# Optimization experiments

Measured on AMD Instinct MI355X. Metric: run time of the kernel, lower is better.

## Reference

```python
import jax, jax.numpy as jnp
import numpy as np

EMD_DIM = 64
NB_EMD = 512


def setup_inputs() -> dict:
    key = jax.random.key(0)
    k_x, k_e = jax.random.split(key)
    x = jax.random.normal(k_x, (32, 64, 64, EMD_DIM), dtype=jnp.float32)
    # codebook buffer, shape [emd_dim, nb_emd] as in the torch module
    embed = jax.random.normal(k_e, (EMD_DIM, NB_EMD), dtype=jnp.float32)
    return {"x": x, "embed": embed}


def reference(x, embed):
    # Eval-mode forward (the EMA buffer update only runs under self.training
    # and does not affect this forward's outputs).
    flatten = x.reshape(-1, EMD_DIM)                      # [N, d]
    dist = (jnp.sum(flatten * flatten, axis=1, keepdims=True)
            - 2.0 * flatten @ embed
            + jnp.sum(embed * embed, axis=0, keepdims=True))  # [N, K]
    emd_id_flat = jnp.argmax(-dist, axis=1)               # nearest code index [N]
    emd_id = emd_id_flat.reshape(x.shape[:-1])            # [B, H, W]
    q = jnp.take(embed.T, emd_id, axis=0)                 # gather codes -> [B,H,W,d]
    diff = jnp.mean((jax.lax.stop_gradient(q) - x) ** 2)  # commitment loss
    q_st = x + jax.lax.stop_gradient(q - x)               # straight-through
    return (q_st, diff, emd_id)
```

## Files before the change

kernel.cpp:

```cpp
#include <hip/hip_runtime.h>

#define N_VEC 131072
#define D 64
#define K 512
#define GUARD 0.05f
#define NB_GATHER 2048
#define FB_Q 16

typedef __attribute__((ext_vector_type(8))) short bf16x8;
typedef __attribute__((ext_vector_type(4))) float f32x4;

static __device__ __forceinline__ short f2bf(float f) {
  unsigned u = __builtin_bit_cast(unsigned, f);
  u += 0x7fffu + ((u >> 16) & 1u);
  return (short)(u >> 16);
}
static __device__ __forceinline__ float bf2f(short h) {
  unsigned u = ((unsigned)(unsigned short)h) << 16;
  return __builtin_bit_cast(float, u);
}
static __device__ __forceinline__ void split8(const float4 f0, const float4 f1,
                                              bf16x8& h, bf16x8& m) {
  const float v[8] = {f0.x, f0.y, f0.z, f0.w, f1.x, f1.y, f1.z, f1.w};
#pragma unroll
  for (int j = 0; j < 8; ++j) {
    const short hh = f2bf(v[j]);
    h[j] = hh;
    m[j] = f2bf(v[j] - bf2f(hh));
  }
}

__global__ __launch_bounds__(64) void vq_prep_kernel(
    const float* __restrict__ embed, float* __restrict__ et,
    float* __restrict__ nrm, bf16x8* __restrict__ F, int* __restrict__ cnt)
{
  const int b = blockIdx.x;
  const int lane = threadIdx.x;
  if (b < 32) {
    const int row = lane & 15;
    const int kg  = lane >> 4;
    const int code = b * 16 + row;
#pragma unroll
    for (int c = 0; c < 2; ++c) {
      bf16x8 h, m;
#pragma unroll
      for (int j = 0; j < 8; ++j) {
        const int d = kg * 8 + c * 32 + j;
        const float e = embed[d * K + code];
        const short hh = f2bf(e);
        h[j] = hh;
        m[j] = f2bf(e - bf2f(hh));
      }
      F[b * 256 + c * 128 + 0  + lane] = h;
      F[b * 256 + c * 128 + 64 + lane] = m;
    }
  } else {
    if (b == 32 && lane == 0) cnt[0] = 0;
    const int code = (b - 32) * 64 + lane;
    float s = 0.f;
#pragma unroll
    for (int d = 0; d < D; ++d) {
      const float e = embed[d * K + code];
      et[code * D + d] = e;
      s = fmaf(e, e, s);
    }
    nrm[code] = s;
  }
}

__global__ __launch_bounds__(64, 4) void vq_coarse_kernel(
    const float* __restrict__ x, const bf16x8* __restrict__ F,
    const float* __restrict__ nrm, float* __restrict__ idf,
    int* __restrict__ cnt, int* __restrict__ list)
{
  const int lane = threadIdx.x;
  const int wid  = blockIdx.x;
  const int qbase = wid * 32;
  const int row = lane & 15;
  const int kg  = lane >> 4;

  bf16x8 Ah0c0, Ah0c1, Ah1c0, Ah1c1, Am0c0, Am0c1, Am1c0, Am1c1;
  {
    const float* xr0 = x + (size_t)(qbase + row) * D + kg * 8;
    const float* xr1 = x + (size_t)(qbase + 16 + row) * D + kg * 8;
    split8(*reinterpret_cast<const float4*>(xr0),
           *reinterpret_cast<const float4*>(xr0 + 4), Ah0c0, Am0c0);
    split8(*reinterpret_cast<const float4*>(xr0 + 32),
           *reinterpret_cast<const float4*>(xr0 + 36), Ah0c1, Am0c1);
    split8(*reinterpret_cast<const float4*>(xr1),
           *reinterpret_cast<const float4*>(xr1 + 4), Ah1c0, Am1c0);
    split8(*reinterpret_cast<const float4*>(xr1 + 32),
           *reinterpret_cast<const float4*>(xr1 + 36), Ah1c1, Am1c1);
  }

  float b1[8], b2[8]; int i1[8];
#pragma unroll
  for (int r = 0; r < 8; ++r) { b1[r] = 3.4e38f; b2[r] = 3.4e38f; i1[r] = 0; }

  const bf16x8* fp = F + lane;
  bf16x8 Bh0 = fp[0], Bm0 = fp[64], Bh1 = fp[128], Bm1 = fp[192];
  fp += 256;
  const float* np = nrm + row;
  float nv = np[0];
  np += 16;

#pragma unroll 1
  for (int t = 0; t < 32; ++t) {
    bf16x8 nh0, nm0, nh1, nm1; float nvn;
    if (t < 31) {
      nh0 = fp[0]; nm0 = fp[64]; nh1 = fp[128]; nm1 = fp[192]; fp += 256;
      nvn = np[0]; np += 16;
    }

    f32x4 p0 = {0.f,0.f,0.f,0.f}, q0 = {0.f,0.f,0.f,0.f};
    f32x4 p1 = {0.f,0.f,0.f,0.f}, q1 = {0.f,0.f,0.f,0.f};
    p0 = __builtin_amdgcn_mfma_f32_16x16x32_bf16(Ah0c0, Bh0, p0, 0, 0, 0);
    p1 = __builtin_amdgcn_mfma_f32_16x16x32_bf16(Ah1c0, Bh0, p1, 0, 0, 0);
    q0 = __builtin_amdgcn_mfma_f32_16x16x32_bf16(Ah0c1, Bm1, q0, 0, 0, 0);
    q1 = __builtin_amdgcn_mfma_f32_16x16x32_bf16(Ah1c1, Bm1, q1, 0, 0, 0);
    p0 = __builtin_amdgcn_mfma_f32_16x16x32_bf16(Ah0c1, Bh1, p0, 0, 0, 0);
    p1 = __builtin_amdgcn_mfma_f32_16x16x32_bf16(Ah1c1, Bh1, p1, 0, 0, 0);
    q0 = __builtin_amdgcn_mfma_f32_16x16x32_bf16(Am0c0, Bh0, q0, 0, 0, 0);
    q1 = __builtin_amdgcn_mfma_f32_16x16x32_bf16(Am1c0, Bh0, q1, 0, 0, 0);
    p0 = __builtin_amdgcn_mfma_f32_16x16x32_bf16(Ah0c0, Bm0, p0, 0, 0, 0);
    p1 = __builtin_amdgcn_mfma_f32_16x16x32_bf16(Ah1c0, Bm0, p1, 0, 0, 0);
    q0 = __builtin_amdgcn_mfma_f32_16x16x32_bf16(Am0c1, Bh1, q0, 0, 0, 0);
    q1 = __builtin_amdgcn_mfma_f32_16x16x32_bf16(Am1c1, Bh1, q1, 0, 0, 0);

    const int code = t * 16 + row;
#pragma unroll
    for (int r = 0; r < 4; ++r) {
      const float s0 = fmaf(-2.f, p0[r], fmaf(-2.f, q0[r], nv));
      b2[r] = __builtin_amdgcn_fmed3f(s0, b1[r], b2[r]);
      if (s0 < b1[r]) { b1[r] = s0; i1[r] = code; }
      const float s1 = fmaf(-2.f, p1[r], fmaf(-2.f, q1[r], nv));
      b2[4 + r] = __builtin_amdgcn_fmed3f(s1, b1[4 + r], b2[4 + r]);
      if (s1 < b1[4 + r]) { b1[4 + r] = s1; i1[4 + r] = code; }
    }
    Bh0 = nh0; Bm0 = nm0; Bh1 = nh1; Bm1 = nm1; nv = nvn;
  }

#pragma unroll
  for (int m = 1; m < 16; m <<= 1) {
#pragma unroll
    for (int r = 0; r < 8; ++r) {
      const float o1 = __shfl_xor(b1[r], m, 64);
      const int   oi = __shfl_xor(i1[r], m, 64);
      const float o2 = __shfl_xor(b2[r], m, 64);
      if (o1 < b1[r]) { b2[r] = fminf(b1[r], o2); b1[r] = o1; i1[r] = oi; }
      else            { b2[r] = fminf(b2[r], o1); }
    }
  }

  unsigned m32 = 0;
  if (row == 0) {
#pragma unroll
    for (int r = 0; r < 8; ++r) {
      const int qoff = (r >> 2) * 16 + kg * 4 + (r & 3);
      idf[qbase + qoff] = (float)i1[r];
      if (b2[r] - b1[r] < GUARD) m32 |= 1u << qoff;
    }
  }
  m32 |= __shfl_xor((int)m32, 16, 64);
  m32 |= __shfl_xor((int)m32, 32, 64);
  if (lane == 0 && m32) {
    int base = atomicAdd(cnt, __popc(m32));
    while (m32) {
      const int b = __ffs(m32) - 1;
      m32 &= m32 - 1;
      list[base++] = qbase + b;
    }
  }
}

__global__ __launch_bounds__(256) void vq_fallback_kernel(
    const float* __restrict__ x, const float* __restrict__ embed,
    const float* __restrict__ nrm, const int* __restrict__ cnt,
    const int* __restrict__ list, float* __restrict__ idf)
{
  __shared__ float x_lds[FB_Q * D];
  __shared__ int   s_qidx[FB_Q];
  __shared__ float s_best[4][FB_Q];
  __shared__ int   s_bid[4][FB_Q];
  const int tid  = threadIdx.x;
  const int lane = tid & 63;
  const int wv   = tid >> 6;
  const int n = cnt[0];

  for (int qb = blockIdx.x * FB_Q; qb < n; qb += gridDim.x * FB_Q) {
    __syncthreads();
    if (tid < FB_Q) {
      const int idx = qb + tid;
      s_qidx[tid] = list[idx < n ? idx : qb];
    }
    __syncthreads();
    {
      const int qj = tid >> 4, dq = tid & 15;
      *reinterpret_cast<float4*>(&x_lds[qj * D + dq * 4]) =
          *reinterpret_cast<const float4*>(x + (size_t)s_qidx[qj] * D + dq * 4);
    }
    __syncthreads();

    const int c0 = wv * 128 + lane;
    const int c1 = c0 + 64;
    float a0[FB_Q], a1[FB_Q];
#pragma unroll
    for (int i = 0; i < FB_Q; ++i) { a0[i] = 0.f; a1[i] = 0.f; }

#pragma unroll 4
    for (int ch = 0; ch < 16; ++ch) {
      const int d0 = ch * 4;
      const float e00 = embed[(d0 + 0) * K + c0];
      const float e01 = embed[(d0 + 0) * K + c1];
      const float e10 = embed[(d0 + 1) * K + c0];
      const float e11 = embed[(d0 + 1) * K + c1];
      const float e20 = embed[(d0 + 2) * K + c0];
      const float e21 = embed[(d0 + 2) * K + c1];
      const float e30 = embed[(d0 + 3) * K + c0];
      const float e31 = embed[(d0 + 3) * K + c1];
#pragma unroll
      for (int i = 0; i < FB_Q; ++i) {
        const float4 xv = *reinterpret_cast<const float4*>(&x_lds[i * D + d0]);
        a0[i] = fmaf(xv.x, e00, a0[i]);
        a0[i] = fmaf(xv.y, e10, a0[i]);
        a0[i] = fmaf(xv.z, e20, a0[i]);
        a0[i] = fmaf(xv.w, e30, a0[i]);
        a1[i] = fmaf(xv.x, e01, a1[i]);
        a1[i] = fmaf(xv.y, e11, a1[i]);
        a1[i] = fmaf(xv.z, e21, a1[i]);
        a1[i] = fmaf(xv.w, e31, a1[i]);
      }
    }

    const float nr0 = nrm[c0], nr1 = nrm[c1];
#pragma unroll
    for (int i = 0; i < FB_Q; ++i) {
      float best; int bid;
      const float s0 = fmaf(-2.f, a0[i], nr0);
      best = s0; bid = c0;
      const float s1 = fmaf(-2.f, a1[i], nr1);
      if (s1 < best) { best = s1; bid = c1; }
#pragma unroll
      for (int off = 32; off > 0; off >>= 1) {
        const float s2 = __shfl_down(best, off, 64);
        const int   b2 = __shfl_down(bid, off, 64);
        if (s2 < best || (s2 == best && b2 < bid)) { best = s2; bid = b2; }
      }
      if (lane == 0) { s_best[wv][i] = best; s_bid[wv][i] = bid; }
    }
    __syncthreads();
    if (tid < FB_Q) {
      float best = s_best[0][tid]; int bid = s_bid[0][tid];
#pragma unroll
      for (int w = 1; w < 4; ++w) {
        const float s = s_best[w][tid];
        if (s < best) { best = s; bid = s_bid[w][tid]; }
      }
      idf[s_qidx[tid]] = (float)bid;
    }
  }
}

__global__ __launch_bounds__(256) void vq_gather_kernel(
    const float* __restrict__ x, const float* __restrict__ et,
    const float* __restrict__ idf, float* __restrict__ q,
    float* __restrict__ partial)
{
  const int tid = blockIdx.x * 256 + threadIdx.x;
  const int stride = gridDim.x * 256;
  float acc = 0.f;
  for (int idx = tid; idx < N_VEC * (D / 4); idx += stride) {
    const int v = idx >> 4;
    const int d4 = idx & 15;
    const int id = (int)idf[v];
    const float4 xv = reinterpret_cast<const float4*>(x)[idx];
    const float4 ev = reinterpret_cast<const float4*>(et)[(id << 4) + d4];
    const float e0 = ev.x - xv.x, e1 = ev.y - xv.y, e2 = ev.z - xv.z, e3 = ev.w - xv.w;
    acc += (e0 * e0 + e1 * e1) + (e2 * e2 + e3 * e3);
    reinterpret_cast<float4*>(q)[idx] = ev;
  }
  acc += __shfl_down(acc, 32, 64);
  acc += __shfl_down(acc, 16, 64);
  acc += __shfl_down(acc, 8, 64);
  acc += __shfl_down(acc, 4, 64);
  acc += __shfl_down(acc, 2, 64);
  acc += __shfl_down(acc, 1, 64);
  __shared__ float sred[4];
  if ((threadIdx.x & 63) == 0) sred[threadIdx.x >> 6] = acc;
  __syncthreads();
  if (threadIdx.x == 0)
    partial[blockIdx.x] = (sred[0] + sred[1]) + (sred[2] + sred[3]);
}

__global__ __launch_bounds__(256) void vq_finalize_kernel(
    const float* __restrict__ partial, float* __restrict__ out)
{
  float acc = 0.f;
  for (int i = threadIdx.x; i < NB_GATHER; i += 256) acc += partial[i];
  acc += __shfl_down(acc, 32, 64);
  acc += __shfl_down(acc, 16, 64);
  acc += __shfl_down(acc, 8, 64);
  acc += __shfl_down(acc, 4, 64);
  acc += __shfl_down(acc, 2, 64);
  acc += __shfl_down(acc, 1, 64);
  __shared__ float sred[4];
  if ((threadIdx.x & 63) == 0) sred[threadIdx.x >> 6] = acc;
  __syncthreads();
  if (threadIdx.x == 0)
    out[0] = ((sred[0] + sred[1]) + (sred[2] + sred[3])) * (1.0f / (float)(N_VEC * D));
}

extern "C" void kernel_launch(void* const* d_in, const int* in_sizes, int n_in,
                              void* d_out, int out_size, void* d_ws, size_t ws_size,
                              hipStream_t stream) {
  const float* x = (const float*)d_in[0];
  const float* embed = (const float*)d_in[1];
  float* out = (float*)d_out;
  float* q    = out;
  float* diff = out + 8388608;
  float* idf  = out + 8388609;

  float* ws = (float*)d_ws;
  float* et      = ws;
  float* nrm     = ws + 32768;
  float* partial = ws + 33280;
  int*   cnt     = (int*)(ws + 35328);
  int*   list    = (int*)(ws + 35336);
  bf16x8* F = (bf16x8*)(ws + 35336 + N_VEC);

  vq_prep_kernel<<<40, 64, 0, stream>>>(embed, et, nrm, F, cnt);
  vq_coarse_kernel<<<N_VEC / 32, 64, 0, stream>>>(x, F, nrm, idf, cnt, list);
  vq_fallback_kernel<<<1024, 256, 0, stream>>>(x, embed, nrm, cnt, list, idf);
  vq_gather_kernel<<<NB_GATHER, 256, 0, stream>>>(x, et, idf, q, partial);
  vq_finalize_kernel<<<1, 256, 0, stream>>>(partial, diff);
}
```

Baseline: 84.67 us.

## Software-pipeline coarse MFMA distance tiles with double-buffered accumulators

The coarse search loop is unrolled by two, with two sets of accumulators and codebook fragment registers. The MFMAs for the next 16-code tile are issued while the VALU scores and updates the top-2 for the previous tile, so matrix-core latency overlaps the compare work instead of serialising with it. Register pressure rises, so launch bounds are lowered from 4 to 3 waves per SIMD. The workspace offsets after nrm are shifted, and the last iteration prefetches one tile past the end of F, which reads harmlessly into the workspace.

```diff
diff --git a/kernel.cpp b/kernel.cpp
--- a/kernel.cpp
+++ b/kernel.cpp
@@ -68,7 +68,38 @@
   }
 }
 
-__global__ __launch_bounds__(64, 4) void vq_coarse_kernel(
+#define MFMA12(P0, Q0, P1, Q1, BH0, BM0, BH1, BM1) do {                        \
+    P0 = __builtin_amdgcn_mfma_f32_16x16x32_bf16(Ah0c0, BH0, kZero, 0, 0, 0); \
+    P1 = __builtin_amdgcn_mfma_f32_16x16x32_bf16(Ah1c0, BH0, kZero, 0, 0, 0); \
+    Q0 = __builtin_amdgcn_mfma_f32_16x16x32_bf16(Ah0c1, BM1, kZero, 0, 0, 0); \
+    Q1 = __builtin_amdgcn_mfma_f32_16x16x32_bf16(Ah1c1, BM1, kZero, 0, 0, 0); \
+    P0 = __builtin_amdgcn_mfma_f32_16x16x32_bf16(Ah0c1, BH1, P0, 0, 0, 0);    \
+    P1 = __builtin_amdgcn_mfma_f32_16x16x32_bf16(Ah1c1, BH1, P1, 0, 0, 0);    \
+    Q0 = __builtin_amdgcn_mfma_f32_16x16x32_bf16(Am0c0, BH0, Q0, 0, 0, 0);    \
+    Q1 = __builtin_amdgcn_mfma_f32_16x16x32_bf16(Am1c0, BH0, Q1, 0, 0, 0);    \
+    P0 = __builtin_amdgcn_mfma_f32_16x16x32_bf16(Ah0c0, BM0, P0, 0, 0, 0);    \
+    P1 = __builtin_amdgcn_mfma_f32_16x16x32_bf16(Ah1c0, BM0, P1, 0, 0, 0);    \
+    Q0 = __builtin_amdgcn_mfma_f32_16x16x32_bf16(Am0c1, BH1, Q0, 0, 0, 0);    \
+    Q1 = __builtin_amdgcn_mfma_f32_16x16x32_bf16(Am1c1, BH1, Q1, 0, 0, 0);    \
+  } while (0)
+
+#define SCORE4(P0, Q0, P1, Q1, CODE, NV) do {                                  \
+    _Pragma("unroll")                                                          \
+    for (int r = 0; r < 4; ++r) {                                              \
+      const float s0 = fmaf(-2.f, P0[r], fmaf(-2.f, Q0[r], (NV)));             \
+      b2[r] = __builtin_amdgcn_fmed3f(s0, b1[r], b2[r]);                       \
+      if (s0 < b1[r]) { b1[r] = s0; i1[r] = (CODE); }                          \
+      const float s1 = fmaf(-2.f, P1[r], fmaf(-2.f, Q1[r], (NV)));             \
+      b2[4 + r] = __builtin_amdgcn_fmed3f(s1, b1[4 + r], b2[4 + r]);           \
+      if (s1 < b1[4 + r]) { b1[4 + r] = s1; i1[4 + r] = (CODE); }              \
+    }                                                                          \
+  } while (0)
+
+#define LOADB(BH0, BM0, BH1, BM1, PTR) do {                                    \
+    BH0 = (PTR)[0]; BM0 = (PTR)[64]; BH1 = (PTR)[128]; BM1 = (PTR)[192];       \
+  } while (0)
+
+__global__ __launch_bounds__(64, 3) void vq_coarse_kernel(
     const float* __restrict__ x, const bf16x8* __restrict__ F,
     const float* __restrict__ nrm, float* __restrict__ idf,
     int* __restrict__ cnt, int* __restrict__ list)
@@ -97,48 +128,42 @@
 #pragma unroll
   for (int r = 0; r < 8; ++r) { b1[r] = 3.4e38f; b2[r] = 3.4e38f; i1[r] = 0; }
 
+  const f32x4 kZero = {0.f, 0.f, 0.f, 0.f};
+  bf16x8 X0h0, X0m0, X0h1, X0m1;
+  bf16x8 X1h0, X1m0, X1h1, X1m1;
+  f32x4 pA0, qA0, pA1, qA1;
+  f32x4 pB0, qB0, pB1, qB1;
+
   const bf16x8* fp = F + lane;
-  bf16x8 Bh0 = fp[0], Bm0 = fp[64], Bh1 = fp[128], Bm1 = fp[192];
+  const float* np = nrm + row;
+
+  float nvA  = np[0];
+  float nvBc = np[16];
+  np += 32;
+  LOADB(X0h0, X0m0, X0h1, X0m1, fp);
+  LOADB(X1h0, X1m0, X1h1, X1m1, fp + 256);
+  fp += 512;
+  MFMA12(pA0, qA0, pA1, qA1, X0h0, X0m0, X0h1, X0m1);
+  LOADB(X0h0, X0m0, X0h1, X0m1, fp);
   fp += 256;
-  const float* np = nrm + row;
-  float nv = np[0];
-  np += 16;
+  MFMA12(pB0, qB0, pB1, qB1, X1h0, X1m0, X1h1, X1m1);
+  SCORE4(pA0, qA0, pA1, qA1, row, nvA);
 
 #pragma unroll 1
-  for (int t = 0; t < 32; ++t) {
-    bf16x8 nh0, nm0, nh1, nm1; float nvn;
-    if (t < 31) {
-      nh0 = fp[0]; nm0 = fp[64]; nh1 = fp[128]; nm1 = fp[192]; fp += 256;
-      nvn = np[0]; np += 16;
-    }
-
-    f32x4 p0 = {0.f,0.f,0.f,0.f}, q0 = {0.f,0.f,0.f,0.f};
-    f32x4 p1 = {0.f,0.f,0.f,0.f}, q1 = {0.f,0.f,0.f,0.f};
-    p0 = __builtin_amdgcn_mfma_f32_16x16x32_bf16(Ah0c0, Bh0, p0, 0, 0, 0);
-    p1 = __builtin_amdgcn_mfma_f32_16x16x32_bf16(Ah1c0, Bh0, p1, 0, 0, 0);
-    q0 = __builtin_amdgcn_mfma_f32_16x16x32_bf16(Ah0c1, Bm1, q0, 0, 0, 0);
-    q1 = __builtin_amdgcn_mfma_f32_16x16x32_bf16(Ah1c1, Bm1, q1, 0, 0, 0);
-    p0 = __builtin_amdgcn_mfma_f32_16x16x32_bf16(Ah0c1, Bh1, p0, 0, 0, 0);
-    p1 = __builtin_amdgcn_mfma_f32_16x16x32_bf16(Ah1c1, Bh1, p1, 0, 0, 0);
-    q0 = __builtin_amdgcn_mfma_f32_16x16x32_bf16(Am0c0, Bh0, q0, 0, 0, 0);
-    q1 = __builtin_amdgcn_mfma_f32_16x16x32_bf16(Am1c0, Bh0, q1, 0, 0, 0);
-    p0 = __builtin_amdgcn_mfma_f32_16x16x32_bf16(Ah0c0, Bm0, p0, 0, 0, 0);
-    p1 = __builtin_amdgcn_mfma_f32_16x16x32_bf16(Ah1c0, Bm0, p1, 0, 0, 0);
-    q0 = __builtin_amdgcn_mfma_f32_16x16x32_bf16(Am0c1, Bh1, q0, 0, 0, 0);
-    q1 = __builtin_amdgcn_mfma_f32_16x16x32_bf16(Am1c1, Bh1, q1, 0, 0, 0);
-
-    const int code = t * 16 + row;
-#pragma unroll
-    for (int r = 0; r < 4; ++r) {
-      const float s0 = fmaf(-2.f, p0[r], fmaf(-2.f, q0[r], nv));
-      b2[r] = __builtin_amdgcn_fmed3f(s0, b1[r], b2[r]);
-      if (s0 < b1[r]) { b1[r] = s0; i1[r] = code; }
-      const float s1 = fmaf(-2.f, p1[r], fmaf(-2.f, q1[r], nv));
-      b2[4 + r] = __builtin_amdgcn_fmed3f(s1, b1[4 + r], b2[4 + r]);
-      if (s1 < b1[4 + r]) { b1[4 + r] = s1; i1[4 + r] = code; }
-    }
-    Bh0 = nh0; Bm0 = nm0; Bh1 = nh1; Bm1 = nm1; nv = nvn;
-  }
+  for (int tp = 2; tp <= 30; tp += 2) {
+    const float nvA2 = np[0];
+    const float nvB  = np[16];
+    np += 32;
+    LOADB(X1h0, X1m0, X1h1, X1m1, fp);
+    MFMA12(pA0, qA0, pA1, qA1, X0h0, X0m0, X0h1, X0m1);
+    SCORE4(pB0, qB0, pB1, qB1, (tp - 1) * 16 + row, nvBc);
+    LOADB(X0h0, X0m0, X0h1, X0m1, fp + 256);
+    fp += 512;
+    MFMA12(pB0, qB0, pB1, qB1, X1h0, X1m0, X1h1, X1m1);
+    SCORE4(pA0, qA0, pA1, qA1, tp * 16 + row, nvA2);
+    nvBc = nvB;
+  }
+  SCORE4(pB0, qB0, pB1, qB1, 31 * 16 + row, nvBc);
 
 #pragma unroll
   for (int m = 1; m < 16; m <<= 1) {
@@ -323,10 +348,10 @@
   float* ws = (float*)d_ws;
   float* et      = ws;
   float* nrm     = ws + 32768;
-  float* partial = ws + 33280;
-  int*   cnt     = (int*)(ws + 35328);
-  int*   list    = (int*)(ws + 35336);
-  bf16x8* F = (bf16x8*)(ws + 35336 + N_VEC);
+  float* partial = ws + 33312;
+  int*   cnt     = (int*)(ws + 35360);
+  int*   list    = (int*)(ws + 35368);
+  bf16x8* F = (bf16x8*)(ws + 35368 + N_VEC);
 
   vq_prep_kernel<<<40, 64, 0, stream>>>(embed, et, nrm, F, cnt);
   vq_coarse_kernel<<<N_VEC / 32, 64, 0, stream>>>(x, F, nrm, idf, cnt, list);
```

Measured after the change: 83.86 us. About the same (-0.9%).
